# Performance work log

Measured on AMD Instinct MI355X. Metric: run time of the kernel, lower is better.

The kernel has to match this reference:

```python
import jax, jax.numpy as jnp
import numpy as np


def setup_inputs() -> dict:
    key = jax.random.key(0)
    ks = jax.random.split(key, 8)
    B, C, H, W = 4, 256, 64, 64
    x = jax.random.normal(ks[0], (B, C, H, W), dtype=jnp.float32)
    y = jax.random.normal(ks[1], (B, C, H, W), dtype=jnp.float32)
    s = 1.0 / np.sqrt(C)
    Wq = jax.random.normal(ks[2], (C, C), dtype=jnp.float32) * s
    bq = jax.random.normal(ks[3], (C,), dtype=jnp.float32) * 0.02
    Wk = jax.random.normal(ks[4], (C, C), dtype=jnp.float32) * s
    bk = jax.random.normal(ks[5], (C,), dtype=jnp.float32) * 0.02
    Wv = jax.random.normal(ks[6], (C, C), dtype=jnp.float32) * s
    bv = jax.random.normal(ks[7], (C,), dtype=jnp.float32) * 0.02
    return {"x": x, "y": y, "Wq": Wq, "bq": bq, "Wk": Wk, "bk": bk, "Wv": Wv, "bv": bv}


def reference(x, y, Wq, bq, Wk, bk, Wv, bv):
    B, C, H, W = x.shape
    scale = C ** (-0.5)
    # flatten spatial dims: [B, N, C] with N = H*W
    x_flat = x.reshape(B, C, H * W).transpose(0, 2, 1)
    y_flat = y.reshape(B, C, H * W).transpose(0, 2, 1)
    # linear projections (torch Linear: x @ W.T + b)
    Q = jnp.einsum('bnc,dc->bnd', x_flat, Wq) + bq
    K = jnp.einsum('bnc,dc->bnd', y_flat, Wk) + bk
    V = jnp.einsum('bnc,dc->bnd', y_flat, Wv) + bv
    # single-head full cross-attention
    scores = jnp.einsum('bqd,bkd->bqk', Q, K) * scale  # [B, N, N]
    attn = jax.nn.softmax(scores, axis=-1)
    out = jnp.einsum('bqk,bkd->bqd', attn, V)  # [B, N, C]
    out = out.transpose(0, 2, 1).reshape(B, C, H, W)
    return x + out
```

## Files before the change

### kernel.cpp

```cpp
#include <hip/hip_runtime.h>
#include <stdint.h>

#define BN 4
#define CD 256
#define ND 4096
#define NK 32
#define WPK_M 65536

typedef unsigned short u16;
typedef short bfrag __attribute__((ext_vector_type(8)));
typedef float ffrag __attribute__((ext_vector_type(4)));

__device__ __forceinline__ float bf2f(u16 u) {
  union { unsigned int i; float f; } v;
  v.i = ((unsigned int)u) << 16;
  return v.f;
}
__device__ __forceinline__ u16 f2bf(float f) {
  union { float f; unsigned int i; } v;
  v.f = f;
  return (u16)((v.i + 0x7FFFu + ((v.i >> 16) & 1u)) >> 16);
}
__device__ __forceinline__ unsigned int cvtpk(float a, float b) {
  unsigned int r;
  asm("v_cvt_pk_bf16_f32 %0, %1, %2" : "=v"(r) : "v"(a), "v"(b));
  return r;
}
__device__ __forceinline__ void gload_lds(const u16* g, u16* l) {
  __builtin_amdgcn_global_load_lds(
      (const __attribute__((address_space(1))) void*)g,
      (__attribute__((address_space(3))) void*)l, 16, 0, 0);
}

__global__ __launch_bounds__(256) void k_packW(
    const float* __restrict__ Wq, const float* __restrict__ Wk,
    const float* __restrict__ Wv, u16* __restrict__ Wpk) {
  int idx = blockIdx.x * 256 + threadIdx.x;
  int lane = idx & 63;
  int fb = idx >> 6;
  int nt = fb & 15, kc = (fb >> 4) & 7, m = fb >> 7;
  const float* W = (m == 0) ? Wq : ((m == 1) ? Wk : Wv);
  const float* s = W + (size_t)(nt * 16 + (lane & 15)) * CD + kc * 32 + (lane >> 4) * 8;
  u16* d = Wpk + (size_t)m * WPK_M + ((size_t)(kc * 16 + nt)) * 512 + lane * 8;
  float4 v0 = *(const float4*)(s);
  float4 v1 = *(const float4*)(s + 4);
  ushort4 o0, o1;
  o0.x = f2bf(v0.x); o0.y = f2bf(v0.y); o0.z = f2bf(v0.z); o0.w = f2bf(v0.w);
  o1.x = f2bf(v1.x); o1.y = f2bf(v1.y); o1.z = f2bf(v1.z); o1.w = f2bf(v1.w);
  *(ushort4*)(d) = o0;
  *(ushort4*)(d + 4) = o1;
}

__global__ __launch_bounds__(256, 4) void k_proj3(
    const float* __restrict__ x, const float* __restrict__ y,
    const u16* __restrict__ Wpk, const float* __restrict__ bq,
    const float* __restrict__ bk, const float* __restrict__ bv,
    u16* __restrict__ Qb, u16* __restrict__ Kb, u16* __restrict__ Vb) {
  __shared__ alignas(16) union {
    u16 S1[64][264];
    u16 Vt[256][72];
  } sm;
  int t = threadIdx.x, w = t >> 6, l = t & 63;
  int lane16 = l & 15, quad = l >> 4;
  int zz = blockIdx.z;

  if (zz < 2) {
    int m0 = (blockIdx.y * 64 + blockIdx.x) * 64;
    int b = m0 >> 12, nsp = m0 & 4095;
    const float* src = (zz ? y : x) + (size_t)b * CD * ND;
    const float* bias = zz ? bk : bq;
    u16* Cd = (zz ? Kb : Qb) + (size_t)m0 * CD;
    const u16* Wz = Wpk + (size_t)zz * WPK_M;

    {
      int u = t & 15, grp = t >> 4;
#pragma unroll
      for (int it = 0; it < 8; ++it) {
        int c = it * 32 + grp * 2;
        const float* col0 = src + (size_t)c * ND + nsp;
        const float* col1 = col0 + ND;
#pragma unroll
        for (int j = 0; j < 4; ++j) {
          int row = j * 16 + u;
          unsigned int pk = cvtpk(col0[row], col1[row]);
          *(unsigned int*)&sm.S1[row][c] = pk;
        }
      }
    }
    __syncthreads();

    bfrag af[8];
#pragma unroll
    for (int kc = 0; kc < 8; ++kc)
      af[kc] = *(const bfrag*)&sm.S1[w * 16 + lane16][kc * 32 + quad * 8];

    ffrag acc[16];
#pragma unroll
    for (int i = 0; i < 16; ++i) acc[i] = ffrag{0.f, 0.f, 0.f, 0.f};

#pragma unroll
    for (int kc = 0; kc < 8; ++kc) {
      const u16* base = Wz + ((size_t)kc * 16) * 512 + l * 8;
#pragma unroll
      for (int nt = 0; nt < 16; ++nt) {
        bfrag bfr = *(const bfrag*)(base + nt * 512);
        acc[nt] = __builtin_amdgcn_mfma_f32_16x16x32_bf16(af[kc], bfr, acc[nt], 0, 0, 0);
      }
    }
    __syncthreads();
#pragma unroll
    for (int nt = 0; nt < 16; ++nt) {
      int col = nt * 16 + lane16;
      float bcol = bias[col];
      unsigned int p01 = cvtpk(acc[nt][0] + bcol, acc[nt][1] + bcol);
      unsigned int p23 = cvtpk(acc[nt][2] + bcol, acc[nt][3] + bcol);
      int r0 = w * 16 + quad * 4;
      sm.S1[r0 + 0][col] = (u16)p01;
      sm.S1[r0 + 1][col] = (u16)(p01 >> 16);
      sm.S1[r0 + 2][col] = (u16)p23;
      sm.S1[r0 + 3][col] = (u16)(p23 >> 16);
    }
    __syncthreads();
#pragma unroll
    for (int it = 0; it < 8; ++it) {
      int i = it * 256 + t;
      int row = i >> 5, chunk = i & 31;
      *(uint4*)(Cd + (size_t)row * CD + chunk * 8) =
          *(const uint4*)&sm.S1[row][chunk * 8];
    }
  } else {
    int n0s = blockIdx.x * 64;
    int b = blockIdx.y;
    const float* src = y + (size_t)b * CD * ND;
    u16* Cd = Vb + (size_t)b * CD * ND;
    const u16* Wz = Wpk + (size_t)2 * WPK_M;

    {
      int u = t & 15, grp = t >> 4;
#pragma unroll
      for (int it = 0; it < 8; ++it) {
        int c = it * 32 + grp * 2;
        const float* col0 = src + (size_t)c * ND + n0s;
        const float* col1 = col0 + ND;
#pragma unroll
        for (int j = 0; j < 4; ++j) {
          int row = j * 16 + u;
          unsigned int pk = cvtpk(col0[row], col1[row]);
          *(unsigned int*)&sm.S1[row][c] = pk;
        }
      }
    }
    __syncthreads();

    bfrag bfr8[8];
#pragma unroll
    for (int kc = 0; kc < 8; ++kc)
      bfr8[kc] = *(const bfrag*)&sm.S1[w * 16 + lane16][kc * 32 + quad * 8];

    ffrag o[16];
#pragma unroll
    for (int i = 0; i < 16; ++i) o[i] = ffrag{0.f, 0.f, 0.f, 0.f};

#pragma unroll
    for (int kc = 0; kc < 8; ++kc) {
      const u16* base = Wz + ((size_t)kc * 16) * 512 + l * 8;
#pragma unroll
      for (int mt = 0; mt < 16; ++mt) {
        bfrag af = *(const bfrag*)(base + mt * 512);
        o[mt] = __builtin_amdgcn_mfma_f32_16x16x32_bf16(af, bfr8[kc], o[mt], 0, 0, 0);
      }
    }
    __syncthreads();
#pragma unroll
    for (int mt = 0; mt < 16; ++mt) {
      int d0 = mt * 16 + quad * 4;
      unsigned int p01 = cvtpk(o[mt][0] + bv[d0 + 0], o[mt][1] + bv[d0 + 1]);
      unsigned int p23 = cvtpk(o[mt][2] + bv[d0 + 2], o[mt][3] + bv[d0 + 3]);
      int nloc = w * 16 + lane16;
      sm.Vt[d0 + 0][nloc] = (u16)p01;
      sm.Vt[d0 + 1][nloc] = (u16)(p01 >> 16);
      sm.Vt[d0 + 2][nloc] = (u16)p23;
      sm.Vt[d0 + 3][nloc] = (u16)(p23 >> 16);
    }
    __syncthreads();
#pragma unroll
    for (int it = 0; it < 8; ++it) {
      int i = it * 256 + t;
      int d = i >> 3, off = (i & 7) * 8;
      *(uint4*)(Cd + (size_t)d * ND + n0s + off) =
          *(const uint4*)&sm.Vt[d][off];
    }
  }
}

union SmemU {
  struct {
    u16 Ks[2][NK][256];
    u16 Vs[2][CD][NK];
    u16 Ps[8][16][36];
  } a;
  u16 ot[CD][136];
};

template <int NS>
__global__ __launch_bounds__(256, 2) void k_attn(
    const u16* __restrict__ Q, const u16* __restrict__ K,
    const u16* __restrict__ Vt, u16* __restrict__ O01,
    u16* __restrict__ O23, float* __restrict__ Lpart) {
  constexpr int NIT = ND / NS / NK;
  constexpr int NBZ = BN * NS;
  __shared__ alignas(16) SmemU sm;
  int lid = blockIdx.x + 32 * (blockIdx.y + BN * blockIdx.z);
  int xcd = lid & 7, j = lid >> 3;
  int bz, qt;
  if (NBZ == 16) { bz = (xcd << 1) | (j & 1); qt = j >> 1; }
  else           { bz = xcd;                  qt = j; }
  int b = bz & (BN - 1), z = bz >> 2;
  int q0 = qt * 128;
  int t = threadIdx.x, w = t >> 6, l = t & 63;
  int lane16 = l & 15, quad = l >> 4;
  const float scale = 0.0625f;

  bfrag qf[2][8];
#pragma unroll
  for (int mi = 0; mi < 2; ++mi) {
    const u16* Qrow =
        Q + ((size_t)b * ND + q0 + (w * 2 + mi) * 16 + lane16) * CD;
#pragma unroll
    for (int kc = 0; kc < 8; ++kc)
      qf[mi][kc] = *(const bfrag*)(Qrow + kc * 32 + quad * 8);
  }

  ffrag o[2][16];
#pragma unroll
  for (int mi = 0; mi < 2; ++mi)
#pragma unroll
    for (int i = 0; i < 16; ++i) o[mi][i] = ffrag{0.f, 0.f, 0.f, 0.f};
  float lsum[2][4] = {{0.f, 0.f, 0.f, 0.f}, {0.f, 0.f, 0.f, 0.f}};

  const u16* Kb = K + ((size_t)b * ND + z * (ND / NS)) * CD;
  const u16* Vb = Vt + (size_t)b * CD * ND + z * (ND / NS);

  auto stage = [&](int kt2) {
    int dbuf = kt2 & 1;
    const u16* Kt = Kb + (size_t)kt2 * NK * CD;
    const u16* Vtt = Vb + kt2 * NK;
#pragma unroll
    for (int p = 0; p < 4; ++p) {
      int r = p * 8 + w * 2 + (l >> 5);
      int jj = (l & 31) ^ (r & 7);
      gload_lds(Kt + (size_t)r * CD + jj * 8, &sm.a.Ks[dbuf][p * 8 + w * 2][0]);
    }
#pragma unroll
    for (int p = 0; p < 4; ++p) {
      int dd = p * 64 + w * 16 + (l >> 2);
      int jj = (l & 3) ^ ((dd >> 1) & 3);
      gload_lds(Vtt + (size_t)dd * ND + jj * 8, &sm.a.Vs[dbuf][p * 64 + w * 16][0]);
    }
  };

  stage(0);
  for (int kt = 0; kt < NIT; ++kt) {
    int dbuf = kt & 1;
    __syncthreads();
    if (kt + 1 < NIT) stage(kt + 1);

    ffrag s2[2][2];
#pragma unroll
    for (int mi = 0; mi < 2; ++mi)
#pragma unroll
      for (int tt = 0; tt < 2; ++tt) s2[mi][tt] = ffrag{0.f, 0.f, 0.f, 0.f};
#pragma unroll
    for (int kc = 0; kc < 8; ++kc) {
      bfrag kf0, kf1;
      {
        int r = lane16;
        int cp = (kc * 4 + quad) ^ (r & 7);
        kf0 = *(const bfrag*)&sm.a.Ks[dbuf][r][cp * 8];
        int r1 = 16 + lane16;
        int cp1 = (kc * 4 + quad) ^ (r1 & 7);
        kf1 = *(const bfrag*)&sm.a.Ks[dbuf][r1][cp1 * 8];
      }
#pragma unroll
      for (int mi = 0; mi < 2; ++mi) {
        s2[mi][0] = __builtin_amdgcn_mfma_f32_16x16x32_bf16(qf[mi][kc], kf0,
                                                            s2[mi][0], 0, 0, 0);
        s2[mi][1] = __builtin_amdgcn_mfma_f32_16x16x32_bf16(qf[mi][kc], kf1,
                                                            s2[mi][1], 0, 0, 0);
      }
    }

#pragma unroll
    for (int mi = 0; mi < 2; ++mi)
#pragma unroll
      for (int tt = 0; tt < 2; ++tt)
#pragma unroll
        for (int r = 0; r < 4; ++r) {
          float p = __expf(s2[mi][tt][r] * scale);
          lsum[mi][r] += p;
          sm.a.Ps[w * 2 + mi][quad * 4 + r][tt * 16 + lane16] = f2bf(p);
        }
    bfrag pf0 = *(const bfrag*)&sm.a.Ps[w * 2 + 0][lane16][quad * 8];
    bfrag pf1 = *(const bfrag*)&sm.a.Ps[w * 2 + 1][lane16][quad * 8];

#pragma unroll
    for (int dt = 0; dt < 16; ++dt) {
      int dd = dt * 16 + lane16;
      int cp = quad ^ ((dd >> 1) & 3);
      bfrag vf = *(const bfrag*)&sm.a.Vs[dbuf][dd][cp * 8];
      o[0][dt] = __builtin_amdgcn_mfma_f32_16x16x32_bf16(pf0, vf, o[0][dt], 0, 0, 0);
      o[1][dt] = __builtin_amdgcn_mfma_f32_16x16x32_bf16(pf1, vf, o[1][dt], 0, 0, 0);
    }
  }

#pragma unroll
  for (int mi = 0; mi < 2; ++mi)
#pragma unroll
    for (int r = 0; r < 4; ++r) {
#pragma unroll
      for (int off = 1; off < 16; off <<= 1)
        lsum[mi][r] += __shfl_xor(lsum[mi][r], off, 64);
    }
  if (lane16 == 0) {
#pragma unroll
    for (int mi = 0; mi < 2; ++mi)
#pragma unroll
      for (int r = 0; r < 4; ++r)
        Lpart[((size_t)z * BN + b) * ND + q0 + (w * 2 + mi) * 16 + quad * 4 + r] =
            lsum[mi][r];
  }

  __syncthreads();
#pragma unroll
  for (int mi = 0; mi < 2; ++mi)
#pragma unroll
    for (int dt = 0; dt < 16; ++dt)
#pragma unroll
      for (int r = 0; r < 4; ++r)
        sm.ot[dt * 16 + lane16][(w * 2 + mi) * 16 + quad * 4 + r] =
            f2bf(o[mi][dt][r]);
  __syncthreads();
  const size_t SZc = (size_t)BN * ND * CD;
  u16* Op = ((z < 2) ? O01 : O23) + (size_t)(z & 1) * SZc;
#pragma unroll
  for (int it = 0; it < 16; ++it) {
    int c = it * 256 + t;
    int dd = c >> 4, co = (c & 15) * 8;
    size_t g = ((size_t)b * CD + dd) * ND + q0 + co;
    *(uint4*)(Op + g) = *(const uint4*)&sm.ot[dd][co];
  }
}

template <int NS>
__global__ __launch_bounds__(256) void k_combine(
    const u16* __restrict__ O01, const u16* __restrict__ O23,
    const float* __restrict__ L, const float* __restrict__ x,
    float* __restrict__ out) {
  const size_t SZc = (size_t)BN * ND * CD;
  size_t e = ((size_t)blockIdx.x * 256 + threadIdx.x) * 8;
  int n = (int)(e & (ND - 1));
  int b = (int)(e >> 20);
  float ls[8] = {0, 0, 0, 0, 0, 0, 0, 0};
  float acc[8] = {0, 0, 0, 0, 0, 0, 0, 0};
#pragma unroll
  for (int z = 0; z < NS; ++z) {
    const float* Lr = L + ((size_t)z * BN + b) * ND + n;
    float4 l0 = *(const float4*)(Lr);
    float4 l1 = *(const float4*)(Lr + 4);
    ls[0] += l0.x; ls[1] += l0.y; ls[2] += l0.z; ls[3] += l0.w;
    ls[4] += l1.x; ls[5] += l1.y; ls[6] += l1.z; ls[7] += l1.w;
    const u16* Oz = ((z < 2) ? O01 : O23) + (size_t)(z & 1) * SZc + e;
    union { uint4 q; u16 s[8]; } u;
    u.q = *(const uint4*)Oz;
#pragma unroll
    for (int j = 0; j < 8; ++j) acc[j] += bf2f(u.s[j]);
  }
  float4 x0 = *(const float4*)(x + e);
  float4 x1 = *(const float4*)(x + e + 4);
  float4 r0, r1;
  r0.x = x0.x + acc[0] / ls[0];
  r0.y = x0.y + acc[1] / ls[1];
  r0.z = x0.z + acc[2] / ls[2];
  r0.w = x0.w + acc[3] / ls[3];
  r1.x = x1.x + acc[4] / ls[4];
  r1.y = x1.y + acc[5] / ls[5];
  r1.z = x1.z + acc[6] / ls[6];
  r1.w = x1.w + acc[7] / ls[7];
  *(float4*)(out + e) = r0;
  *(float4*)(out + e + 4) = r1;
}

extern "C" void kernel_launch(void* const* d_in, const int* in_sizes, int n_in,
                              void* d_out, int out_size, void* d_ws, size_t ws_size,
                              hipStream_t stream) {
  const float* x  = (const float*)d_in[0];
  const float* y  = (const float*)d_in[1];
  const float* Wq = (const float*)d_in[2];
  const float* bq = (const float*)d_in[3];
  const float* Wk = (const float*)d_in[4];
  const float* bk = (const float*)d_in[5];
  const float* Wv = (const float*)d_in[6];
  const float* bv = (const float*)d_in[7];
  float* out = (float*)d_out;
  u16* ws = (u16*)d_ws;
  const size_t SZ = (size_t)BN * ND * CD;
  u16* Qb = ws;
  u16* Kb = Qb + SZ;
  u16* Vb = Kb + SZ;
  u16* Ob = Vb + SZ;
  const size_t need4 = 7 * SZ * sizeof(u16) +
                       (size_t)4 * BN * ND * sizeof(float) +
                       (size_t)3 * WPK_M * sizeof(u16);
  const bool big = ws_size >= need4;
  const int cgrid = (int)(SZ / (256 * 8));

  if (big) {
    float* Lp = (float*)(Ob + 4 * SZ);
    u16* Wpk = (u16*)(Lp + (size_t)4 * BN * ND);
    k_packW<<<dim3(96), 256, 0, stream>>>(Wq, Wk, Wv, Wpk);
    k_proj3<<<dim3(64, 4, 3), 256, 0, stream>>>(x, y, Wpk, bq, bk, bv,
                                                Qb, Kb, Vb);
    k_attn<4><<<dim3(ND / 128, BN, 4), 256, 0, stream>>>(Qb, Kb, Vb, Ob,
                                                         Ob + 2 * SZ, Lp);
    k_combine<4><<<dim3(cgrid), 256, 0, stream>>>(Ob, Ob + 2 * SZ, Lp, x, out);
  } else {
    float* Lp = (float*)(Ob + 2 * SZ);
    u16* Wpk = (u16*)(Lp + (size_t)2 * BN * ND);
    k_packW<<<dim3(96), 256, 0, stream>>>(Wq, Wk, Wv, Wpk);
    k_proj3<<<dim3(64, 4, 3), 256, 0, stream>>>(x, y, Wpk, bq, bk, bv,
                                                Qb, Kb, Vb);
    k_attn<2><<<dim3(ND / 128, BN, 2), 256, 0, stream>>>(Qb, Kb, Vb, Ob, Ob, Lp);
    k_combine<2><<<dim3(cgrid), 256, 0, stream>>>(Ob, Ob, Lp, x, out);
  }
}
```

Measured before the change: 191.7 us.

## Split attention block across 8 waves with one 16-row query tile each

The attention kernel now launches 512 threads per block, and each of 8 waves handles one 16-row query tile instead of two. This halves the per-thread accumulator and Q-fragment registers, allowing launch bounds of 4 blocks per CU for more latency hiding. In exchange, each K/V fragment loaded from shared memory feeds only one MFMA instead of two, raising LDS traffic per flop. The block-wide syncs now span more waves.

```diff
diff --git a/kernel.cpp b/kernel.cpp
--- a/kernel.cpp
+++ b/kernel.cpp
@@ -203,7 +203,7 @@
 };
 
 template <int NS>
-__global__ __launch_bounds__(256, 2) void k_attn(
+__global__ __launch_bounds__(512, 4) void k_attn(
     const u16* __restrict__ Q, const u16* __restrict__ K,
     const u16* __restrict__ Vt, u16* __restrict__ O01,
     u16* __restrict__ O23, float* __restrict__ Lpart) {
@@ -221,22 +221,18 @@
   int lane16 = l & 15, quad = l >> 4;
   const float scale = 0.0625f;
 
-  bfrag qf[2][8];
-#pragma unroll
-  for (int mi = 0; mi < 2; ++mi) {
-    const u16* Qrow =
-        Q + ((size_t)b * ND + q0 + (w * 2 + mi) * 16 + lane16) * CD;
+  bfrag qf[8];
+  {
+    const u16* Qrow = Q + ((size_t)b * ND + q0 + w * 16 + lane16) * CD;
 #pragma unroll
     for (int kc = 0; kc < 8; ++kc)
-      qf[mi][kc] = *(const bfrag*)(Qrow + kc * 32 + quad * 8);
-  }
-
-  ffrag o[2][16];
-#pragma unroll
-  for (int mi = 0; mi < 2; ++mi)
-#pragma unroll
-    for (int i = 0; i < 16; ++i) o[mi][i] = ffrag{0.f, 0.f, 0.f, 0.f};
-  float lsum[2][4] = {{0.f, 0.f, 0.f, 0.f}, {0.f, 0.f, 0.f, 0.f}};
+      qf[kc] = *(const bfrag*)(Qrow + kc * 32 + quad * 8);
+  }
+
+  ffrag o[16];
+#pragma unroll
+  for (int i = 0; i < 16; ++i) o[i] = ffrag{0.f, 0.f, 0.f, 0.f};
+  float lsum[4] = {0.f, 0.f, 0.f, 0.f};
 
   const u16* Kb = K + ((size_t)b * ND + z * (ND / NS)) * CD;
   const u16* Vb = Vt + (size_t)b * CD * ND + z * (ND / NS);
@@ -246,16 +242,16 @@
     const u16* Kt = Kb + (size_t)kt2 * NK * CD;
     const u16* Vtt = Vb + kt2 * NK;
 #pragma unroll
-    for (int p = 0; p < 4; ++p) {
-      int r = p * 8 + w * 2 + (l >> 5);
+    for (int p = 0; p < 2; ++p) {
+      int r = p * 16 + w * 2 + (l >> 5);
       int jj = (l & 31) ^ (r & 7);
-      gload_lds(Kt + (size_t)r * CD + jj * 8, &sm.a.Ks[dbuf][p * 8 + w * 2][0]);
-    }
-#pragma unroll
-    for (int p = 0; p < 4; ++p) {
-      int dd = p * 64 + w * 16 + (l >> 2);
+      gload_lds(Kt + (size_t)r * CD + jj * 8, &sm.a.Ks[dbuf][p * 16 + w * 2][0]);
+    }
+#pragma unroll
+    for (int p = 0; p < 2; ++p) {
+      int dd = p * 128 + w * 16 + (l >> 2);
       int jj = (l & 3) ^ ((dd >> 1) & 3);
-      gload_lds(Vtt + (size_t)dd * ND + jj * 8, &sm.a.Vs[dbuf][p * 64 + w * 16][0]);
+      gload_lds(Vtt + (size_t)dd * ND + jj * 8, &sm.a.Vs[dbuf][p * 128 + w * 16][0]);
     }
   };
 
@@ -265,86 +261,61 @@
     __syncthreads();
     if (kt + 1 < NIT) stage(kt + 1);
 
-    ffrag s2[2][2];
-#pragma unroll
-    for (int mi = 0; mi < 2; ++mi)
-#pragma unroll
-      for (int tt = 0; tt < 2; ++tt) s2[mi][tt] = ffrag{0.f, 0.f, 0.f, 0.f};
+    ffrag s2[2];
+    s2[0] = ffrag{0.f, 0.f, 0.f, 0.f};
+    s2[1] = ffrag{0.f, 0.f, 0.f, 0.f};
 #pragma unroll
     for (int kc = 0; kc < 8; ++kc) {
-      bfrag kf0, kf1;
-      {
-        int r = lane16;
-        int cp = (kc * 4 + quad) ^ (r & 7);
-        kf0 = *(const bfrag*)&sm.a.Ks[dbuf][r][cp * 8];
-        int r1 = 16 + lane16;
-        int cp1 = (kc * 4 + quad) ^ (r1 & 7);
-        kf1 = *(const bfrag*)&sm.a.Ks[dbuf][r1][cp1 * 8];
+      int cp = (kc * 4 + quad) ^ (lane16 & 7);
+      bfrag kf0 = *(const bfrag*)&sm.a.Ks[dbuf][lane16][cp * 8];
+      bfrag kf1 = *(const bfrag*)&sm.a.Ks[dbuf][16 + lane16][cp * 8];
+      s2[0] = __builtin_amdgcn_mfma_f32_16x16x32_bf16(qf[kc], kf0, s2[0], 0, 0, 0);
+      s2[1] = __builtin_amdgcn_mfma_f32_16x16x32_bf16(qf[kc], kf1, s2[1], 0, 0, 0);
+    }
+
+#pragma unroll
+    for (int tt = 0; tt < 2; ++tt)
+#pragma unroll
+      for (int r = 0; r < 4; ++r) {
+        float p = __expf(s2[tt][r] * scale);
+        lsum[r] += p;
+        sm.a.Ps[w][quad * 4 + r][tt * 16 + lane16] = f2bf(p);
       }
-#pragma unroll
-      for (int mi = 0; mi < 2; ++mi) {
-        s2[mi][0] = __builtin_amdgcn_mfma_f32_16x16x32_bf16(qf[mi][kc], kf0,
-                                                            s2[mi][0], 0, 0, 0);
-        s2[mi][1] = __builtin_amdgcn_mfma_f32_16x16x32_bf16(qf[mi][kc], kf1,
-                                                            s2[mi][1], 0, 0, 0);
-      }
-    }
-
-#pragma unroll
-    for (int mi = 0; mi < 2; ++mi)
-#pragma unroll
-      for (int tt = 0; tt < 2; ++tt)
-#pragma unroll
-        for (int r = 0; r < 4; ++r) {
-          float p = __expf(s2[mi][tt][r] * scale);
-          lsum[mi][r] += p;
-          sm.a.Ps[w * 2 + mi][quad * 4 + r][tt * 16 + lane16] = f2bf(p);
-        }
-    bfrag pf0 = *(const bfrag*)&sm.a.Ps[w * 2 + 0][lane16][quad * 8];
-    bfrag pf1 = *(const bfrag*)&sm.a.Ps[w * 2 + 1][lane16][quad * 8];
+    bfrag pf = *(const bfrag*)&sm.a.Ps[w][lane16][quad * 8];
 
 #pragma unroll
     for (int dt = 0; dt < 16; ++dt) {
       int dd = dt * 16 + lane16;
       int cp = quad ^ ((dd >> 1) & 3);
       bfrag vf = *(const bfrag*)&sm.a.Vs[dbuf][dd][cp * 8];
-      o[0][dt] = __builtin_amdgcn_mfma_f32_16x16x32_bf16(pf0, vf, o[0][dt], 0, 0, 0);
-      o[1][dt] = __builtin_amdgcn_mfma_f32_16x16x32_bf16(pf1, vf, o[1][dt], 0, 0, 0);
-    }
-  }
-
-#pragma unroll
-  for (int mi = 0; mi < 2; ++mi)
-#pragma unroll
-    for (int r = 0; r < 4; ++r) {
-#pragma unroll
-      for (int off = 1; off < 16; off <<= 1)
-        lsum[mi][r] += __shfl_xor(lsum[mi][r], off, 64);
-    }
+      o[dt] = __builtin_amdgcn_mfma_f32_16x16x32_bf16(pf, vf, o[dt], 0, 0, 0);
+    }
+  }
+
+#pragma unroll
+  for (int r = 0; r < 4; ++r) {
+#pragma unroll
+    for (int off = 1; off < 16; off <<= 1)
+      lsum[r] += __shfl_xor(lsum[r], off, 64);
+  }
   if (lane16 == 0) {
 #pragma unroll
-    for (int mi = 0; mi < 2; ++mi)
-#pragma unroll
-      for (int r = 0; r < 4; ++r)
-        Lpart[((size_t)z * BN + b) * ND + q0 + (w * 2 + mi) * 16 + quad * 4 + r] =
-            lsum[mi][r];
+    for (int r = 0; r < 4; ++r)
+      Lpart[((size_t)z * BN + b) * ND + q0 + w * 16 + quad * 4 + r] = lsum[r];
   }
 
   __syncthreads();
 #pragma unroll
-  for (int mi = 0; mi < 2; ++mi)
-#pragma unroll
-    for (int dt = 0; dt < 16; ++dt)
-#pragma unroll
-      for (int r = 0; r < 4; ++r)
-        sm.ot[dt * 16 + lane16][(w * 2 + mi) * 16 + quad * 4 + r] =
-            f2bf(o[mi][dt][r]);
+  for (int dt = 0; dt < 16; ++dt)
+#pragma unroll
+    for (int r = 0; r < 4; ++r)
+      sm.ot[dt * 16 + lane16][w * 16 + quad * 4 + r] = f2bf(o[dt][r]);
   __syncthreads();
   const size_t SZc = (size_t)BN * ND * CD;
   u16* Op = ((z < 2) ? O01 : O23) + (size_t)(z & 1) * SZc;
 #pragma unroll
-  for (int it = 0; it < 16; ++it) {
-    int c = it * 256 + t;
+  for (int it = 0; it < 8; ++it) {
+    int c = it * 512 + t;
     int dd = c >> 4, co = (c & 15) * 8;
     size_t g = ((size_t)b * CD + dd) * ND + q0 + co;
     *(uint4*)(Op + g) = *(const uint4*)&sm.ot[dd][co];
@@ -420,7 +391,7 @@
     k_packW<<<dim3(96), 256, 0, stream>>>(Wq, Wk, Wv, Wpk);
     k_proj3<<<dim3(64, 4, 3), 256, 0, stream>>>(x, y, Wpk, bq, bk, bv,
                                                 Qb, Kb, Vb);
-    k_attn<4><<<dim3(ND / 128, BN, 4), 256, 0, stream>>>(Qb, Kb, Vb, Ob,
+    k_attn<4><<<dim3(ND / 128, BN, 4), 512, 0, stream>>>(Qb, Kb, Vb, Ob,
                                                          Ob + 2 * SZ, Lp);
     k_combine<4><<<dim3(cgrid), 256, 0, stream>>>(Ob, Ob + 2 * SZ, Lp, x, out);
   } else {
@@ -429,7 +400,7 @@
     k_packW<<<dim3(96), 256, 0, stream>>>(Wq, Wk, Wv, Wpk);
     k_proj3<<<dim3(64, 4, 3), 256, 0, stream>>>(x, y, Wpk, bq, bk, bv,
                                                 Qb, Kb, Vb);
-    k_attn<2><<<dim3(ND / 128, BN, 2), 256, 0, stream>>>(Qb, Kb, Vb, Ob, Ob, Lp);
+    k_attn<2><<<dim3(ND / 128, BN, 2), 512, 0, stream>>>(Qb, Kb, Vb, Ob, Ob, Lp);
     k_combine<2><<<dim3(cgrid), 256, 0, stream>>>(Ob, Ob, Lp, x, out);
   }
 }
```

Result: slower. 214.4 us (+11.8%).
